# Kernel tuning notes

Measured on AMD Instinct MI355X. Metric: run time of the kernel, lower is better.

## Reference

```python
import jax, jax.numpy as jnp
import numpy as np

K = 5            # adaptive kernel size
C = 256          # inplanes
M = 4
CM = C // M      # 64 bottleneck channels
PLANES = 256


def _depthwise_per_sample(f, w, b, dilation, pad):
    # f: [N, Cm, H, W]; w: [N, Cm, kh, kw] per-sample depthwise weights; b: [Cm]
    # Fold batch into the channel/group dim so one grouped conv does all samples.
    N, Cm, H, W = f.shape
    x = f.reshape(1, N * Cm, H, W)
    wk = w.reshape(N * Cm, 1, w.shape[2], w.shape[3])
    out = jax.lax.conv_general_dilated(
        x, wk, window_strides=(1, 1), padding=[(pad, pad), (pad, pad)],
        rhs_dilation=(dilation, dilation), feature_group_count=N * Cm,
        dimension_numbers=("NCHW", "OIHW", "NCHW"))
    return out.reshape(N, Cm, H, W) + b[None, :, None, None]


def setup_inputs() -> dict:
    key = jax.random.key(0)
    ks = jax.random.split(key, 16)
    N, H, W = 16, 96, 96
    s = 0.05
    return {
        "x": jax.random.normal(ks[0], (N, C, H, W), jnp.float32),
        "conv_w": jax.random.normal(ks[1], (CM, C)) * s,            # 1x1 conv C->Cm
        "conv_b": jax.random.normal(ks[2], (CM,)) * s,
        "conv_k_w": jax.random.normal(ks[3], ()) * s + 1.0,          # conv_k: 1x1, 1ch
        "conv_k_b": jax.random.normal(ks[4], ()) * s,
        "conv_k2_w": jax.random.normal(ks[5], ()) * s + 1.0,         # conv_k2
        "conv_k2_b": jax.random.normal(ks[6], ()) * s,
        "conv_kernel_w": jax.random.normal(ks[7], (K * K,)) * s,     # 1 -> k*k
        "conv_kernel_b": jax.random.normal(ks[8], (K * K,)) * s,
        "conv_kernel2_w": jax.random.normal(ks[9], (9,)) * s,        # 1 -> 9
        "conv_kernel2_b": jax.random.normal(ks[10], (9,)) * s,
        "fuse_w": jax.random.normal(ks[11], (PLANES // 2, CM)) * s,  # 1x1 fuse
        "fuse_b": jax.random.normal(ks[12], (PLANES // 2,)) * s,
        "adap_b": jax.random.normal(ks[13], (CM,)) * s,              # conv_adap_kernel.bias
        "atrous_b": jax.random.normal(ks[14], (CM,)) * s,            # conv3x3_atrous bias
    }


def reference(x, conv_w, conv_b, conv_k_w, conv_k_b, conv_k2_w, conv_k2_b,
              conv_kernel_w, conv_kernel_b, conv_kernel2_w, conv_kernel2_b,
              fuse_w, fuse_b, adap_b, atrous_b):
    N = x.shape[0]
    # f = relu(1x1 conv)
    f = jax.nn.relu(jnp.einsum("oc,nchw->nohw", conv_w, x) + conv_b[None, :, None, None])
    # g = relu(conv(avg_pool(x))) -> [N, Cm]
    g = jax.nn.relu(x.mean(axis=(2, 3)) @ conv_w.T + conv_b)
    # conv_kernel (1->k*k, 1x1) applied over the Cm "spatial" axis, then conv_k (scalar affine)
    # kernel[n,c,kk] = conv_k_w * (conv_kernel_w[kk]*g[n,c] + conv_kernel_b[kk]) + conv_k_b
    ker = conv_k_w * (g[:, :, None] * conv_kernel_w[None, None, :] + conv_kernel_b) + conv_k_b
    w_dyn = ker.reshape(N, CM, K, K)
    ker2 = conv_k2_w * (g[:, :, None] * conv_kernel2_w[None, None, :] + conv_kernel2_b) + conv_k2_b
    w_atr = ker2.reshape(N, CM, 3, 3)
    # per-sample dynamic depthwise convs
    out = _depthwise_per_sample(f, w_dyn, adap_b, dilation=1, pad=(K - 1) // 2)
    out_atr = _depthwise_per_sample(f, w_atr, atrous_b, dilation=2, pad=2)
    # fuse (1x1) each branch, concat on channels
    y = jnp.einsum("oc,nchw->nohw", fuse_w, out) + fuse_b[None, :, None, None]
    y_atr = jnp.einsum("oc,nchw->nohw", fuse_w, out_atr) + fuse_b[None, :, None, None]
    return jnp.concatenate([y, y_atr], axis=1)
```

## Files before the change

### kernel.cpp

```cpp
#include <hip/hip_runtime.h>
#include <hip/hip_bf16.h>
#include <stdint.h>

#define N_S   16
#define C_IN  256
#define CMID  64
#define HH    96
#define WW    96
#define HW    9216
#define PL2   128

#define CB_OFF   0
#define KW_OFF   64
#define KB_OFF   96
#define K2W_OFF  128
#define K2B_OFF  144
#define FB_OFF   160
#define AB_OFF   288
#define ATB_OFF  352
#define SC_OFF   416

typedef __attribute__((ext_vector_type(8))) short short8;
typedef __attribute__((ext_vector_type(4))) float floatx4;

__device__ __forceinline__ float ldbf(const uint16_t* p) {
    return __uint_as_float(((uint32_t)(*p)) << 16);
}
__device__ __forceinline__ uint16_t f2bf(float f) {
    __hip_bfloat16 h = __float2bfloat16(f);
    return *reinterpret_cast<uint16_t*>(&h);
}
__device__ __forceinline__ uint32_t pkbf(float lo, float hi) {
    return (uint32_t)f2bf(lo) | ((uint32_t)f2bf(hi) << 16);
}
__device__ __forceinline__ float bfsum2(uint32_t u) {
    return __uint_as_float(u << 16) + __uint_as_float(u & 0xffff0000u);
}

#define SWZ8(row) ((((row) ^ ((row) >> 3)) & 7) << 3)

__global__ __launch_bounds__(256) void k_prep(
    const uint16_t* __restrict__ xq,
    const void* conv_w, const void* conv_b, const void* ckw, const void* ckb,
    const void* ck2w, const void* ck2b, const void* kernw, const void* kernb,
    const void* kern2w, const void* kern2b, const void* fuse_w, const void* fuse_b,
    const void* adap_b, const void* atrous_b,
    int* __restrict__ flags,
    uint16_t* __restrict__ cw_bf, uint16_t* __restrict__ fw_bf,
    float* __restrict__ smalls) {
    __shared__ int cnt[2];
    int t = threadIdx.x;
    if (t < 2) cnt[t] = 0;
    __syncthreads();
    int cx = 0, cw = 0;
    const uint16_t* wq = (const uint16_t*)conv_w;
    for (int k = 0; k < 64; ++k) {
        uint16_t vx = xq[k * 256 + t];
        uint16_t vw = wq[k * 256 + t];
        if (((vx >> 7) & 0xFF) >= 0xC0) cx++;
        if (((vw >> 7) & 0xFF) >= 0xC0) cw++;
    }
    atomicAdd(&cnt[0], cx);
    atomicAdd(&cnt[1], cw);
    __syncthreads();
    bool f32 = cnt[1] > 64;
    if (blockIdx.x == 0 && t == 0) { flags[0] = cnt[0] > 64; flags[1] = f32; }

    for (int i = blockIdx.x * 256 + t; i < CMID * C_IN; i += 16 * 256)
        cw_bf[i] = f32 ? f2bf(((const float*)conv_w)[i]) : ((const uint16_t*)conv_w)[i];
    for (int i = blockIdx.x * 256 + t; i < PL2 * CMID; i += 16 * 256)
        fw_bf[i] = f32 ? f2bf(((const float*)fuse_w)[i]) : ((const uint16_t*)fuse_w)[i];
    if (blockIdx.x != 0) return;
    if (t < 64) {
        smalls[CB_OFF + t]  = f32 ? ((const float*)conv_b)[t]   : ldbf((const uint16_t*)conv_b + t);
        smalls[AB_OFF + t]  = f32 ? ((const float*)adap_b)[t]   : ldbf((const uint16_t*)adap_b + t);
        smalls[ATB_OFF + t] = f32 ? ((const float*)atrous_b)[t] : ldbf((const uint16_t*)atrous_b + t);
    }
    if (t < 128)
        smalls[FB_OFF + t] = f32 ? ((const float*)fuse_b)[t] : ldbf((const uint16_t*)fuse_b + t);
    if (t < 25) {
        smalls[KW_OFF + t] = f32 ? ((const float*)kernw)[t] : ldbf((const uint16_t*)kernw + t);
        smalls[KB_OFF + t] = f32 ? ((const float*)kernb)[t] : ldbf((const uint16_t*)kernb + t);
    }
    if (t < 9) {
        smalls[K2W_OFF + t] = f32 ? ((const float*)kern2w)[t] : ldbf((const uint16_t*)kern2w + t);
        smalls[K2B_OFF + t] = f32 ? ((const float*)kern2b)[t] : ldbf((const uint16_t*)kern2b + t);
    }
    if (t == 0) {
        smalls[SC_OFF + 0] = f32 ? ((const float*)ckw)[0]  : ldbf((const uint16_t*)ckw);
        smalls[SC_OFF + 1] = f32 ? ((const float*)ckb)[0]  : ldbf((const uint16_t*)ckb);
        smalls[SC_OFF + 2] = f32 ? ((const float*)ck2w)[0] : ldbf((const uint16_t*)ck2w);
        smalls[SC_OFF + 3] = f32 ? ((const float*)ck2b)[0] : ldbf((const uint16_t*)ck2b);
    }
}

__global__ __launch_bounds__(256, 3) void k_conv1x1(
    const void* __restrict__ xv, const int* __restrict__ flags,
    const uint16_t* __restrict__ cw_bf, const float* __restrict__ smalls,
    uint16_t* __restrict__ fout, float* __restrict__ partials) {
    __shared__ uint16_t x_lds[128 * 72];
    int t = threadIdx.x;
    int b = blockIdx.x;
    int n = b / 72, blk = b % 72;
    int pxb = blk * 128;
    bool xf32 = flags[0] != 0;

    int lane = t & 63, wid = t >> 6;
    int l16 = lane & 15, quad = lane >> 4;
    int nb = wid * 32;
    uint32_t* xl32 = (uint32_t*)x_lds;

    floatx4 acc[4][2];
#pragma unroll
    for (int i = 0; i < 4; ++i)
#pragma unroll
        for (int j = 0; j < 2; ++j) acc[i][j] = (floatx4){0.f, 0.f, 0.f, 0.f};

    float* pbase = partials + (size_t)(n * 72 + blk) * 256;

    uint4 st[2][4];

    auto issue = [&](int cc) {
#pragma unroll
        for (int k = 0; k < 2; ++k) {
            int task = k * 256 + t;
            int pxg = task & 15, cp = task >> 4;
            int c = cc * 64 + cp * 2;
            int px0 = pxb + pxg * 8;
            if (xf32) {
                const float* xb = (const float*)xv + ((size_t)n * C_IN + c) * HW + px0;
                st[k][0] = *(const uint4*)xb;
                st[k][1] = *(const uint4*)(xb + 4);
                st[k][2] = *(const uint4*)(xb + HW);
                st[k][3] = *(const uint4*)(xb + HW + 4);
            } else {
                const uint16_t* xb = (const uint16_t*)xv + ((size_t)n * C_IN + c) * HW + px0;
                st[k][0] = *(const uint4*)xb;
                st[k][1] = *(const uint4*)(xb + HW);
            }
        }
    };

    auto convwrite = [&](int cc) {
#pragma unroll
        for (int k = 0; k < 2; ++k) {
            int task = k * 256 + t;
            int pxg = task & 15, cp = task >> 4;
            int c = cc * 64 + cp * 2;
            uint32_t pk[8];
            float s0, s1;
            if (xf32) {
                float av[8], bv[8];
                av[0] = __uint_as_float(st[k][0].x); av[1] = __uint_as_float(st[k][0].y);
                av[2] = __uint_as_float(st[k][0].z); av[3] = __uint_as_float(st[k][0].w);
                av[4] = __uint_as_float(st[k][1].x); av[5] = __uint_as_float(st[k][1].y);
                av[6] = __uint_as_float(st[k][1].z); av[7] = __uint_as_float(st[k][1].w);
                bv[0] = __uint_as_float(st[k][2].x); bv[1] = __uint_as_float(st[k][2].y);
                bv[2] = __uint_as_float(st[k][2].z); bv[3] = __uint_as_float(st[k][2].w);
                bv[4] = __uint_as_float(st[k][3].x); bv[5] = __uint_as_float(st[k][3].y);
                bv[6] = __uint_as_float(st[k][3].z); bv[7] = __uint_as_float(st[k][3].w);
                s0 = ((av[0] + av[1]) + (av[2] + av[3])) + ((av[4] + av[5]) + (av[6] + av[7]));
                s1 = ((bv[0] + bv[1]) + (bv[2] + bv[3])) + ((bv[4] + bv[5]) + (bv[6] + bv[7]));
#pragma unroll
                for (int j = 0; j < 8; ++j) pk[j] = pkbf(av[j], bv[j]);
            } else {
                uint32_t u0[4] = {st[k][0].x, st[k][0].y, st[k][0].z, st[k][0].w};
                uint32_t u1[4] = {st[k][1].x, st[k][1].y, st[k][1].z, st[k][1].w};
                s0 = (bfsum2(u0[0]) + bfsum2(u0[1])) + (bfsum2(u0[2]) + bfsum2(u0[3]));
                s1 = (bfsum2(u1[0]) + bfsum2(u1[1])) + (bfsum2(u1[2]) + bfsum2(u1[3]));
#pragma unroll
                for (int j = 0; j < 8; ++j) {
                    uint32_t lo = (u0[j >> 1] >> ((j & 1) * 16)) & 0xffffu;
                    uint32_t hi = (u1[j >> 1] >> ((j & 1) * 16)) & 0xffffu;
                    pk[j] = lo | (hi << 16);
                }
            }
            int swz = (pxg & 7) << 2;
#pragma unroll
            for (int j = 0; j < 8; ++j)
                xl32[(pxg * 8 + j) * 36 + (cp ^ swz)] = pk[j];
#pragma unroll
            for (int off = 8; off > 0; off >>= 1) {
                s0 += __shfl_xor(s0, off, 16);
                s1 += __shfl_xor(s1, off, 16);
            }
            if ((t & 15) == 0) *(float2*)(pbase + c) = make_float2(s0, s1);
        }
    };

    auto mfma_ph = [&](int cc) {
#pragma unroll
        for (int ks = 0; ks < 2; ++ks) {
            int kw = cc * 64 + ks * 32 + quad * 8;
            const uint16_t* wp = cw_bf + kw;
            short8 a0 = *(const short8*)(wp + (l16)      * 256);
            short8 a1 = *(const short8*)(wp + (16 + l16) * 256);
            short8 a2 = *(const short8*)(wp + (32 + l16) * 256);
            short8 a3 = *(const short8*)(wp + (48 + l16) * 256);
#pragma unroll
            for (int nt = 0; nt < 2; ++nt) {
                int px = nb + nt * 16 + l16;
                int kdw = (ks * 16 + quad * 4) ^ (((px >> 3) & 7) << 2);
                short8 bv = *(const short8*)(xl32 + (size_t)px * 36 + kdw);
                acc[0][nt] = __builtin_amdgcn_mfma_f32_16x16x32_bf16(a0, bv, acc[0][nt], 0, 0, 0);
                acc[1][nt] = __builtin_amdgcn_mfma_f32_16x16x32_bf16(a1, bv, acc[1][nt], 0, 0, 0);
                acc[2][nt] = __builtin_amdgcn_mfma_f32_16x16x32_bf16(a2, bv, acc[2][nt], 0, 0, 0);
                acc[3][nt] = __builtin_amdgcn_mfma_f32_16x16x32_bf16(a3, bv, acc[3][nt], 0, 0, 0);
            }
        }
    };

    issue(0);
    convwrite(0);
    issue(1);
    __syncthreads();
    mfma_ph(0);
    __syncthreads();
    convwrite(1);
    issue(2);
    __syncthreads();
    mfma_ph(1);
    __syncthreads();
    convwrite(2);
    issue(3);
    __syncthreads();
    mfma_ph(2);
    __syncthreads();
    convwrite(3);
    __syncthreads();
    mfma_ph(3);

    __syncthreads();
#pragma unroll
    for (int mt = 0; mt < 4; ++mt) {
        int o = mt * 16 + quad * 4;
        float b0 = smalls[CB_OFF + o],     b1 = smalls[CB_OFF + o + 1];
        float b2 = smalls[CB_OFF + o + 2], b3 = smalls[CB_OFF + o + 3];
#pragma unroll
        for (int nt = 0; nt < 2; ++nt) {
            int pxl = nb + nt * 16 + l16;
            float v0 = fmaxf(acc[mt][nt][0] + b0, 0.f);
            float v1 = fmaxf(acc[mt][nt][1] + b1, 0.f);
            float v2 = fmaxf(acc[mt][nt][2] + b2, 0.f);
            float v3 = fmaxf(acc[mt][nt][3] + b3, 0.f);
            *(uint2*)(x_lds + pxl * 72 + o) = make_uint2(pkbf(v0, v1), pkbf(v2, v3));
        }
    }
    __syncthreads();
#pragma unroll
    for (int k = 0; k < 4; ++k) {
        int task = k * 256 + t;
        int o8 = (task & 7) * 8, pxl = task >> 3;
        *(uint4*)(fout + ((size_t)n * HW + pxb + pxl) * 64 + o8) =
            *(const uint4*)(x_lds + pxl * 72 + o8);
    }
}

__global__ __launch_bounds__(256) void k_weights2(
    const float* __restrict__ partials, const uint16_t* __restrict__ cw_bf,
    const float* __restrict__ smalls,
    float* __restrict__ w_dyn, float* __restrict__ w_atr) {
    __shared__ float s_sums[256];
    __shared__ float s_dot[256];
    int n = blockIdx.x, t = threadIdx.x;
    const float* pp = partials + (size_t)n * 72 * 256 + t;
    float s = 0.f;
#pragma unroll 8
    for (int k = 0; k < 72; ++k) s += pp[k * 256];
    s_sums[t] = s * (1.0f / (float)HW);
    __syncthreads();
    int cm = t & 63, seg = t >> 6;
    const uint16_t* wr = cw_bf + cm * 256 + seg * 64;
    const float* sr = s_sums + seg * 64;
    float acc = 0.f;
#pragma unroll 8
    for (int c = 0; c < 64; ++c) acc = fmaf(ldbf(wr + c), sr[c], acc);
    s_dot[t] = acc;
    __syncthreads();
    if (t < 64) {
        float a = s_dot[t] + s_dot[t + 64] + s_dot[t + 128] + s_dot[t + 192]
                + smalls[CB_OFF + t];
        float gv = fmaxf(a, 0.f);
        float ckw = smalls[SC_OFF + 0], ckb = smalls[SC_OFF + 1];
        float ck2w = smalls[SC_OFF + 2], ck2b = smalls[SC_OFF + 3];
        float* o1 = w_dyn + (size_t)(n * CMID + t) * 25;
#pragma unroll
        for (int k = 0; k < 25; ++k)
            o1[k] = fmaf(ckw, fmaf(gv, smalls[KW_OFF + k], smalls[KB_OFF + k]), ckb);
        float* o2 = w_atr + (size_t)(n * CMID + t) * 9;
#pragma unroll
        for (int k = 0; k < 9; ++k)
            o2[k] = fmaf(ck2w, fmaf(gv, smalls[K2W_OFF + k], smalls[K2B_OFF + k]), ck2b);
    }
}

__global__ __launch_bounds__(256) void k_dwfuse(
    const uint16_t* __restrict__ f,
    const float* __restrict__ w_dyn, const float* __restrict__ w_atr,
    const uint16_t* __restrict__ fw_bf, const float* __restrict__ smalls,
    float* __restrict__ out) {
    __shared__ uint16_t f_lds[160 * 64];
    __shared__ uint16_t d5_lds[64 * 72];
    __shared__ uint16_t dA_lds[64 * 72];

    int t = threadIdx.x;
    int orig = blockIdx.x;
    int b = (orig & 7) * 288 + (orig >> 3);
    int n = b / 144, tile = b % 144;
    int y0 = (tile / 6) * 4, x0 = (tile % 6) * 16;

    int c = t >> 2, q = t & 3;
    int qx = q << 2;
    float w5[25], w9[9];
    {
        const float* wp = w_dyn + (size_t)(n * CMID + c) * 25;
#pragma unroll
        for (int k = 0; k < 25; ++k) w5[k] = wp[k];
        const float* wa = w_atr + (size_t)(n * CMID + c) * 9;
#pragma unroll
        for (int k = 0; k < 9; ++k) w9[k] = wa[k];
    }

    const uint16_t* fbase = f + (size_t)n * HW * 64;
#pragma unroll
    for (int k = 0; k < 5; ++k) {
        int task = k * 256 + t;
        int row = task >> 3, c8 = (task & 7) * 8;
        int hy = row / 20, hx = row - hy * 20;
        int y = y0 - 2 + hy, xg = x0 - 2 + hx;
        uint4 v = make_uint4(0u, 0u, 0u, 0u);
        if (y >= 0 && y < HH && xg >= 0 && xg < WW)
            v = *(const uint4*)(fbase + ((size_t)y * WW + xg) * 64 + c8);
        *(uint4*)(f_lds + row * 64 + (c8 ^ SWZ8(row))) = v;
    }
    __syncthreads();

    {
        float p[8][8];
#pragma unroll
        for (int r = 0; r < 8; ++r)
#pragma unroll
            for (int cl = 0; cl < 8; ++cl) {
                int row = r * 20 + qx + cl;
                p[r][cl] = ldbf(f_lds + row * 64 + (c ^ SWZ8(row)));
            }

        float b5v = smalls[AB_OFF + c], bAv = smalls[ATB_OFF + c];
        float a5[4][4], aA[4][4];
#pragma unroll
        for (int i = 0; i < 4; ++i)
#pragma unroll
            for (int j = 0; j < 4; ++j) { a5[i][j] = b5v; aA[i][j] = bAv; }

#pragma unroll
        for (int i = 0; i < 5; ++i)
#pragma unroll
            for (int j = 0; j < 5; ++j) {
                float wv = w5[i * 5 + j];
#pragma unroll
                for (int oy = 0; oy < 4; ++oy)
#pragma unroll
                    for (int ox = 0; ox < 4; ++ox)
                        a5[oy][ox] = fmaf(wv, p[oy + i][ox + j], a5[oy][ox]);
            }
#pragma unroll
        for (int i = 0; i < 3; ++i)
#pragma unroll
            for (int j = 0; j < 3; ++j) {
                float wv = w9[i * 3 + j];
#pragma unroll
                for (int oy = 0; oy < 4; ++oy)
#pragma unroll
                    for (int ox = 0; ox < 4; ++ox)
                        aA[oy][ox] = fmaf(wv, p[oy + 2 * i][ox + 2 * j], aA[oy][ox]);
            }

#pragma unroll
        for (int oy = 0; oy < 4; ++oy)
#pragma unroll
            for (int ox = 0; ox < 4; ox += 2) {
                int px0 = oy * 16 + qx + ox;
                uint32_t p5 = pkbf(a5[oy][ox], a5[oy][ox + 1]);
                uint32_t pA = pkbf(aA[oy][ox], aA[oy][ox + 1]);
                d5_lds[px0 * 72 + c]       = (uint16_t)p5;
                d5_lds[(px0 + 1) * 72 + c] = (uint16_t)(p5 >> 16);
                dA_lds[px0 * 72 + c]       = (uint16_t)pA;
                dA_lds[(px0 + 1) * 72 + c] = (uint16_t)(pA >> 16);
            }
    }
    __syncthreads();

    {
        int lane = t & 63, wid = t >> 6;
        int l16 = lane & 15, quad = lane >> 4;
        const uint16_t* dl = (wid >= 2) ? dA_lds : d5_lds;
        int oh = (wid & 1) * 64;
        int obr = (wid >= 2) ? 128 : 0;

        floatx4 acc[4][4];
#pragma unroll
        for (int i = 0; i < 4; ++i)
#pragma unroll
            for (int j = 0; j < 4; ++j) acc[i][j] = (floatx4){0.f, 0.f, 0.f, 0.f};

#pragma unroll
        for (int ks = 0; ks < 2; ++ks) {
            int kk = ks * 32 + quad * 8;
            short8 a0 = *(const short8*)(dl + (l16)      * 72 + kk);
            short8 a1 = *(const short8*)(dl + (16 + l16) * 72 + kk);
            short8 a2 = *(const short8*)(dl + (32 + l16) * 72 + kk);
            short8 a3 = *(const short8*)(dl + (48 + l16) * 72 + kk);
#pragma unroll
            for (int nt = 0; nt < 4; ++nt) {
                short8 bv = *(const short8*)(fw_bf + (size_t)(oh + nt * 16 + l16) * 64 + kk);
                acc[0][nt] = __builtin_amdgcn_mfma_f32_16x16x32_bf16(a0, bv, acc[0][nt], 0, 0, 0);
                acc[1][nt] = __builtin_amdgcn_mfma_f32_16x16x32_bf16(a1, bv, acc[1][nt], 0, 0, 0);
                acc[2][nt] = __builtin_amdgcn_mfma_f32_16x16x32_bf16(a2, bv, acc[2][nt], 0, 0, 0);
                acc[3][nt] = __builtin_amdgcn_mfma_f32_16x16x32_bf16(a3, bv, acc[3][nt], 0, 0, 0);
            }
        }
#pragma unroll
        for (int nt = 0; nt < 4; ++nt) {
            int o = oh + nt * 16 + l16;
            float bias = smalls[FB_OFF + o];
            float* obp = out + ((size_t)(n * 256 + obr + o)) * HW + x0 + quad * 4;
#pragma unroll
            for (int mt = 0; mt < 4; ++mt) {
                float4 v;
                v.x = acc[mt][nt][0] + bias;
                v.y = acc[mt][nt][1] + bias;
                v.z = acc[mt][nt][2] + bias;
                v.w = acc[mt][nt][3] + bias;
                *(float4*)(obp + (size_t)(y0 + mt) * WW) = v;
            }
        }
    }
}

extern "C" void kernel_launch(void* const* d_in, const int* in_sizes, int n_in,
                              void* d_out, int out_size, void* d_ws, size_t ws_size,
                              hipStream_t stream) {
    float* out = (float*)d_out;

    char* ws = (char*)d_ws;
    int*      flags = (int*)ws;
    uint16_t* cw_bf = (uint16_t*)(ws + 256);
    uint16_t* fw_bf = (uint16_t*)(ws + 33024);
    float*    smalls = (float*)(ws + 49408);
    float*    partials = (float*)(ws + 65536);
    float*    w_dyn = (float*)(ws + 1245184);
    float*    w_atr = (float*)(ws + 1347584);
    uint16_t* f     = (uint16_t*)(ws + 1384448);

    k_prep<<<dim3(16), dim3(256), 0, stream>>>(
        (const uint16_t*)d_in[0],
        d_in[1], d_in[2], d_in[3], d_in[4], d_in[5], d_in[6], d_in[7], d_in[8],
        d_in[9], d_in[10], d_in[11], d_in[12], d_in[13], d_in[14],
        flags, cw_bf, fw_bf, smalls);
    k_conv1x1<<<dim3(N_S * 72), dim3(256), 0, stream>>>(
        d_in[0], flags, cw_bf, smalls, f, partials);
    k_weights2<<<dim3(N_S), dim3(256), 0, stream>>>(
        partials, cw_bf, smalls, w_dyn, w_atr);
    k_dwfuse<<<dim3(N_S * 144), dim3(256), 0, stream>>>(
        f, w_dyn, w_atr, fw_bf, smalls, out);
}
```

Measured before the change: 393.9 us.

## Halve conv1x1 pixel tile and double-buffer x loads two stages ahead

The 1x1 conv kernel now processes 64 pixels per block instead of 128, doubling the grid to 2304 blocks and dropping the per-wave accumulator set to four MFMA tiles. Loads are issued two channel chunks ahead using two register buffers, so more global memory latency is hidden behind the MFMA phases, and the occupancy hint on launch bounds is removed. The partial-sum buffer doubles in size, so the weights kernel reduces over 144 partials and the workspace offsets shift. The cost is more blocks, more partial-sum writes and more weight reloads per pixel.

New measurement: 368.3 us. 6.5% less time.

```diff
diff --git a/kernel.cpp b/kernel.cpp
--- a/kernel.cpp
+++ b/kernel.cpp
@@ -94,161 +94,141 @@
     }
 }
 
-__global__ __launch_bounds__(256, 3) void k_conv1x1(
+
+#define ISSUE(cc, A0, A1, B0, B1) do {                                          \
+    int c_ = (cc) * 64 + cp * 2;                                                \
+    if (xf32) {                                                                 \
+        const float* xb_ = (const float*)xv + ((size_t)n * C_IN + c_) * HW + px0;\
+        A0 = *(const uint4*)xb_;        A1 = *(const uint4*)(xb_ + 4);          \
+        B0 = *(const uint4*)(xb_ + HW); B1 = *(const uint4*)(xb_ + HW + 4);     \
+    } else {                                                                    \
+        const uint16_t* xb_ = (const uint16_t*)xv + ((size_t)n * C_IN + c_) * HW + px0;\
+        A0 = *(const uint4*)xb_;        B0 = *(const uint4*)(xb_ + HW);         \
+    }                                                                           \
+} while (0)
+
+#define CONVWRITE(cc, A0, A1, B0, B1) do {                                      \
+    int c_ = (cc) * 64 + cp * 2;                                                \
+    uint32_t pk_[8]; float s0_, s1_;                                            \
+    if (xf32) {                                                                 \
+        float av_[8], bw_[8];                                                   \
+        av_[0] = __uint_as_float(A0.x); av_[1] = __uint_as_float(A0.y);         \
+        av_[2] = __uint_as_float(A0.z); av_[3] = __uint_as_float(A0.w);         \
+        av_[4] = __uint_as_float(A1.x); av_[5] = __uint_as_float(A1.y);         \
+        av_[6] = __uint_as_float(A1.z); av_[7] = __uint_as_float(A1.w);         \
+        bw_[0] = __uint_as_float(B0.x); bw_[1] = __uint_as_float(B0.y);         \
+        bw_[2] = __uint_as_float(B0.z); bw_[3] = __uint_as_float(B0.w);         \
+        bw_[4] = __uint_as_float(B1.x); bw_[5] = __uint_as_float(B1.y);         \
+        bw_[6] = __uint_as_float(B1.z); bw_[7] = __uint_as_float(B1.w);         \
+        s0_ = ((av_[0] + av_[1]) + (av_[2] + av_[3]))                           \
+            + ((av_[4] + av_[5]) + (av_[6] + av_[7]));                          \
+        s1_ = ((bw_[0] + bw_[1]) + (bw_[2] + bw_[3]))                           \
+            + ((bw_[4] + bw_[5]) + (bw_[6] + bw_[7]));                          \
+        _Pragma("unroll")                                                       \
+        for (int j = 0; j < 8; ++j) pk_[j] = pkbf(av_[j], bw_[j]);              \
+    } else {                                                                    \
+        s0_ = (bfsum2(A0.x) + bfsum2(A0.y)) + (bfsum2(A0.z) + bfsum2(A0.w));    \
+        s1_ = (bfsum2(B0.x) + bfsum2(B0.y)) + (bfsum2(B0.z) + bfsum2(B0.w));    \
+        pk_[0] = (A0.x & 0xffffu) | (B0.x << 16);                               \
+        pk_[1] = (A0.x >> 16)     | (B0.x & 0xffff0000u);                       \
+        pk_[2] = (A0.y & 0xffffu) | (B0.y << 16);                               \
+        pk_[3] = (A0.y >> 16)     | (B0.y & 0xffff0000u);                       \
+        pk_[4] = (A0.z & 0xffffu) | (B0.z << 16);                               \
+        pk_[5] = (A0.z >> 16)     | (B0.z & 0xffff0000u);                       \
+        pk_[6] = (A0.w & 0xffffu) | (B0.w << 16);                               \
+        pk_[7] = (A0.w >> 16)     | (B0.w & 0xffff0000u);                       \
+    }                                                                           \
+    int swz_ = pxg << 2;                                                        \
+    _Pragma("unroll")                                                           \
+    for (int j = 0; j < 8; ++j)                                                 \
+        xl32[(pxg * 8 + j) * 36 + (cp ^ swz_)] = pk_[j];                        \
+    s0_ += __shfl_xor(s0_, 4, 8); s0_ += __shfl_xor(s0_, 2, 8);                 \
+    s0_ += __shfl_xor(s0_, 1, 8);                                               \
+    s1_ += __shfl_xor(s1_, 4, 8); s1_ += __shfl_xor(s1_, 2, 8);                 \
+    s1_ += __shfl_xor(s1_, 1, 8);                                               \
+    if ((t & 7) == 0) *(float2*)(pbase + c_) = make_float2(s0_, s1_);           \
+} while (0)
+
+#define MFMA_PH(cc) do {                                                        \
+    _Pragma("unroll")                                                           \
+    for (int ks = 0; ks < 2; ++ks) {                                            \
+        int kw_ = (cc) * 64 + ks * 32 + quad * 8;                               \
+        const uint16_t* wp_ = cw_bf + kw_;                                      \
+        short8 a0 = *(const short8*)(wp_ + (l16)      * 256);                   \
+        short8 a1 = *(const short8*)(wp_ + (16 + l16) * 256);                   \
+        short8 a2 = *(const short8*)(wp_ + (32 + l16) * 256);                   \
+        short8 a3 = *(const short8*)(wp_ + (48 + l16) * 256);                   \
+        int kdw_ = (ks * 16 + quad * 4) ^ ((pxw >> 3) << 2);                    \
+        short8 bv = *(const short8*)(xl32 + (size_t)pxw * 36 + kdw_);           \
+        acc[0] = __builtin_amdgcn_mfma_f32_16x16x32_bf16(a0, bv, acc[0], 0, 0, 0);\
+        acc[1] = __builtin_amdgcn_mfma_f32_16x16x32_bf16(a1, bv, acc[1], 0, 0, 0);\
+        acc[2] = __builtin_amdgcn_mfma_f32_16x16x32_bf16(a2, bv, acc[2], 0, 0, 0);\
+        acc[3] = __builtin_amdgcn_mfma_f32_16x16x32_bf16(a3, bv, acc[3], 0, 0, 0);\
+    }                                                                           \
+} while (0)
+
+__global__ __launch_bounds__(256) void k_conv1x1(
     const void* __restrict__ xv, const int* __restrict__ flags,
     const uint16_t* __restrict__ cw_bf, const float* __restrict__ smalls,
     uint16_t* __restrict__ fout, float* __restrict__ partials) {
-    __shared__ uint16_t x_lds[128 * 72];
+    __shared__ uint16_t x_lds[64 * 72];
     int t = threadIdx.x;
     int b = blockIdx.x;
-    int n = b / 72, blk = b % 72;
-    int pxb = blk * 128;
+    int n = b / 144, blk = b % 144;
+    int pxb = blk * 64;
     bool xf32 = flags[0] != 0;
 
     int lane = t & 63, wid = t >> 6;
     int l16 = lane & 15, quad = lane >> 4;
-    int nb = wid * 32;
+    int pxw = wid * 16 + l16;
     uint32_t* xl32 = (uint32_t*)x_lds;
 
-    floatx4 acc[4][2];
-#pragma unroll
-    for (int i = 0; i < 4; ++i)
-#pragma unroll
-        for (int j = 0; j < 2; ++j) acc[i][j] = (floatx4){0.f, 0.f, 0.f, 0.f};
-
-    float* pbase = partials + (size_t)(n * 72 + blk) * 256;
-
-    uint4 st[2][4];
-
-    auto issue = [&](int cc) {
-#pragma unroll
-        for (int k = 0; k < 2; ++k) {
-            int task = k * 256 + t;
-            int pxg = task & 15, cp = task >> 4;
-            int c = cc * 64 + cp * 2;
-            int px0 = pxb + pxg * 8;
-            if (xf32) {
-                const float* xb = (const float*)xv + ((size_t)n * C_IN + c) * HW + px0;
-                st[k][0] = *(const uint4*)xb;
-                st[k][1] = *(const uint4*)(xb + 4);
-                st[k][2] = *(const uint4*)(xb + HW);
-                st[k][3] = *(const uint4*)(xb + HW + 4);
-            } else {
-                const uint16_t* xb = (const uint16_t*)xv + ((size_t)n * C_IN + c) * HW + px0;
-                st[k][0] = *(const uint4*)xb;
-                st[k][1] = *(const uint4*)(xb + HW);
-            }
-        }
-    };
-
-    auto convwrite = [&](int cc) {
-#pragma unroll
-        for (int k = 0; k < 2; ++k) {
-            int task = k * 256 + t;
-            int pxg = task & 15, cp = task >> 4;
-            int c = cc * 64 + cp * 2;
-            uint32_t pk[8];
-            float s0, s1;
-            if (xf32) {
-                float av[8], bv[8];
-                av[0] = __uint_as_float(st[k][0].x); av[1] = __uint_as_float(st[k][0].y);
-                av[2] = __uint_as_float(st[k][0].z); av[3] = __uint_as_float(st[k][0].w);
-                av[4] = __uint_as_float(st[k][1].x); av[5] = __uint_as_float(st[k][1].y);
-                av[6] = __uint_as_float(st[k][1].z); av[7] = __uint_as_float(st[k][1].w);
-                bv[0] = __uint_as_float(st[k][2].x); bv[1] = __uint_as_float(st[k][2].y);
-                bv[2] = __uint_as_float(st[k][2].z); bv[3] = __uint_as_float(st[k][2].w);
-                bv[4] = __uint_as_float(st[k][3].x); bv[5] = __uint_as_float(st[k][3].y);
-                bv[6] = __uint_as_float(st[k][3].z); bv[7] = __uint_as_float(st[k][3].w);
-                s0 = ((av[0] + av[1]) + (av[2] + av[3])) + ((av[4] + av[5]) + (av[6] + av[7]));
-                s1 = ((bv[0] + bv[1]) + (bv[2] + bv[3])) + ((bv[4] + bv[5]) + (bv[6] + bv[7]));
-#pragma unroll
-                for (int j = 0; j < 8; ++j) pk[j] = pkbf(av[j], bv[j]);
-            } else {
-                uint32_t u0[4] = {st[k][0].x, st[k][0].y, st[k][0].z, st[k][0].w};
-                uint32_t u1[4] = {st[k][1].x, st[k][1].y, st[k][1].z, st[k][1].w};
-                s0 = (bfsum2(u0[0]) + bfsum2(u0[1])) + (bfsum2(u0[2]) + bfsum2(u0[3]));
-                s1 = (bfsum2(u1[0]) + bfsum2(u1[1])) + (bfsum2(u1[2]) + bfsum2(u1[3]));
-#pragma unroll
-                for (int j = 0; j < 8; ++j) {
-                    uint32_t lo = (u0[j >> 1] >> ((j & 1) * 16)) & 0xffffu;
-                    uint32_t hi = (u1[j >> 1] >> ((j & 1) * 16)) & 0xffffu;
-                    pk[j] = lo | (hi << 16);
-                }
-            }
-            int swz = (pxg & 7) << 2;
-#pragma unroll
-            for (int j = 0; j < 8; ++j)
-                xl32[(pxg * 8 + j) * 36 + (cp ^ swz)] = pk[j];
-#pragma unroll
-            for (int off = 8; off > 0; off >>= 1) {
-                s0 += __shfl_xor(s0, off, 16);
-                s1 += __shfl_xor(s1, off, 16);
-            }
-            if ((t & 15) == 0) *(float2*)(pbase + c) = make_float2(s0, s1);
-        }
-    };
-
-    auto mfma_ph = [&](int cc) {
-#pragma unroll
-        for (int ks = 0; ks < 2; ++ks) {
-            int kw = cc * 64 + ks * 32 + quad * 8;
-            const uint16_t* wp = cw_bf + kw;
-            short8 a0 = *(const short8*)(wp + (l16)      * 256);
-            short8 a1 = *(const short8*)(wp + (16 + l16) * 256);
-            short8 a2 = *(const short8*)(wp + (32 + l16) * 256);
-            short8 a3 = *(const short8*)(wp + (48 + l16) * 256);
-#pragma unroll
-            for (int nt = 0; nt < 2; ++nt) {
-                int px = nb + nt * 16 + l16;
-                int kdw = (ks * 16 + quad * 4) ^ (((px >> 3) & 7) << 2);
-                short8 bv = *(const short8*)(xl32 + (size_t)px * 36 + kdw);
-                acc[0][nt] = __builtin_amdgcn_mfma_f32_16x16x32_bf16(a0, bv, acc[0][nt], 0, 0, 0);
-                acc[1][nt] = __builtin_amdgcn_mfma_f32_16x16x32_bf16(a1, bv, acc[1][nt], 0, 0, 0);
-                acc[2][nt] = __builtin_amdgcn_mfma_f32_16x16x32_bf16(a2, bv, acc[2][nt], 0, 0, 0);
-                acc[3][nt] = __builtin_amdgcn_mfma_f32_16x16x32_bf16(a3, bv, acc[3][nt], 0, 0, 0);
-            }
-        }
-    };
-
-    issue(0);
-    convwrite(0);
-    issue(1);
-    __syncthreads();
-    mfma_ph(0);
-    __syncthreads();
-    convwrite(1);
-    issue(2);
-    __syncthreads();
-    mfma_ph(1);
-    __syncthreads();
-    convwrite(2);
-    issue(3);
-    __syncthreads();
-    mfma_ph(2);
-    __syncthreads();
-    convwrite(3);
-    __syncthreads();
-    mfma_ph(3);
-
-    __syncthreads();
+    int pxg = t & 7, cp = t >> 3;
+    int px0 = pxb + pxg * 8;
+
+    floatx4 acc[4];
+#pragma unroll
+    for (int i = 0; i < 4; ++i) acc[i] = (floatx4){0.f, 0.f, 0.f, 0.f};
+
+    float* pbase = partials + (size_t)(n * 144 + blk) * 256;
+
+    uint4 pA0, pA1, pB0, pB1;
+    uint4 qA0, qA1, qB0, qB1;
+
+    ISSUE(0, pA0, pA1, pB0, pB1);
+    ISSUE(1, qA0, qA1, qB0, qB1);
+    CONVWRITE(0, pA0, pA1, pB0, pB1);
+    ISSUE(2, pA0, pA1, pB0, pB1);
+    __syncthreads();
+    MFMA_PH(0);
+    __syncthreads();
+    CONVWRITE(1, qA0, qA1, qB0, qB1);
+    ISSUE(3, qA0, qA1, qB0, qB1);
+    __syncthreads();
+    MFMA_PH(1);
+    __syncthreads();
+    CONVWRITE(2, pA0, pA1, pB0, pB1);
+    __syncthreads();
+    MFMA_PH(2);
+    __syncthreads();
+    CONVWRITE(3, qA0, qA1, qB0, qB1);
+    __syncthreads();
+    MFMA_PH(3);
+
 #pragma unroll
     for (int mt = 0; mt < 4; ++mt) {
         int o = mt * 16 + quad * 4;
         float b0 = smalls[CB_OFF + o],     b1 = smalls[CB_OFF + o + 1];
         float b2 = smalls[CB_OFF + o + 2], b3 = smalls[CB_OFF + o + 3];
-#pragma unroll
-        for (int nt = 0; nt < 2; ++nt) {
-            int pxl = nb + nt * 16 + l16;
-            float v0 = fmaxf(acc[mt][nt][0] + b0, 0.f);
-            float v1 = fmaxf(acc[mt][nt][1] + b1, 0.f);
-            float v2 = fmaxf(acc[mt][nt][2] + b2, 0.f);
-            float v3 = fmaxf(acc[mt][nt][3] + b3, 0.f);
-            *(uint2*)(x_lds + pxl * 72 + o) = make_uint2(pkbf(v0, v1), pkbf(v2, v3));
-        }
-    }
-    __syncthreads();
-#pragma unroll
-    for (int k = 0; k < 4; ++k) {
+        float v0 = fmaxf(acc[mt][0] + b0, 0.f);
+        float v1 = fmaxf(acc[mt][1] + b1, 0.f);
+        float v2 = fmaxf(acc[mt][2] + b2, 0.f);
+        float v3 = fmaxf(acc[mt][3] + b3, 0.f);
+        *(uint2*)(x_lds + pxw * 72 + o) = make_uint2(pkbf(v0, v1), pkbf(v2, v3));
+    }
+    __syncthreads();
+#pragma unroll
+    for (int k = 0; k < 2; ++k) {
         int task = k * 256 + t;
         int o8 = (task & 7) * 8, pxl = task >> 3;
         *(uint4*)(fout + ((size_t)n * HW + pxb + pxl) * 64 + o8) =
@@ -263,10 +243,10 @@
     __shared__ float s_sums[256];
     __shared__ float s_dot[256];
     int n = blockIdx.x, t = threadIdx.x;
-    const float* pp = partials + (size_t)n * 72 * 256 + t;
+    const float* pp = partials + (size_t)n * 144 * 256 + t;
     float s = 0.f;
 #pragma unroll 8
-    for (int k = 0; k < 72; ++k) s += pp[k * 256];
+    for (int k = 0; k < 144; ++k) s += pp[k * 256];
     s_sums[t] = s * (1.0f / (float)HW);
     __syncthreads();
     int cm = t & 63, seg = t >> 6;
@@ -448,16 +428,16 @@
     uint16_t* fw_bf = (uint16_t*)(ws + 33024);
     float*    smalls = (float*)(ws + 49408);
     float*    partials = (float*)(ws + 65536);
-    float*    w_dyn = (float*)(ws + 1245184);
-    float*    w_atr = (float*)(ws + 1347584);
-    uint16_t* f     = (uint16_t*)(ws + 1384448);
+    float*    w_dyn = (float*)(ws + 2424832);
+    float*    w_atr = (float*)(ws + 2527232);
+    uint16_t* f     = (uint16_t*)(ws + 2564096);
 
     k_prep<<<dim3(16), dim3(256), 0, stream>>>(
         (const uint16_t*)d_in[0],
         d_in[1], d_in[2], d_in[3], d_in[4], d_in[5], d_in[6], d_in[7], d_in[8],
         d_in[9], d_in[10], d_in[11], d_in[12], d_in[13], d_in[14],
         flags, cw_bf, fw_bf, smalls);
-    k_conv1x1<<<dim3(N_S * 72), dim3(256), 0, stream>>>(
+    k_conv1x1<<<dim3(N_S * 144), dim3(256), 0, stream>>>(
         d_in[0], flags, cw_bf, smalls, f, partials);
     k_weights2<<<dim3(N_S), dim3(256), 0, stream>>>(
         partials, cw_bf, smalls, w_dyn, w_atr);
```
